# Performance work log

Hardware: AMD Instinct MI355X
Metric: run time of the kernel (lower is better)

## Reference

```python
import jax, jax.numpy as jnp
import numpy as np
from jax import lax
import math

DIM = 64
NUM_HEADS = 8
HEAD_SIZE = DIM // NUM_HEADS  # used only for the 1/sqrt scale


def _depth_conv(x, dw, db, pw, pb):
    # x: [B, C, H, W]; dw: [C, 1, 3, 3] depthwise; pw: [C_out, C] pointwise 1x1
    C = x.shape[1]
    y = lax.conv_general_dilated(
        x, dw, window_strides=(1, 1), padding=[(1, 1), (1, 1)],
        dimension_numbers=("NCHW", "OIHW", "NCHW"), feature_group_count=C)
    y = y + db[None, :, None, None]
    y = jnp.einsum("bchw,oc->bohw", y, pw) + pb[None, :, None, None]
    return y


def setup_inputs() -> dict:
    key = jax.random.key(0)
    ks = jax.random.split(key, 14)
    B, C, H, W = 8, DIM, 256, 256
    inp = {
        "hidden_states": jax.random.normal(ks[0], (B, C, H, W), jnp.float32),
        "ctx": jax.random.normal(ks[1], (B, C, H, W), jnp.float32),
    }
    scale_dw = 1.0 / math.sqrt(9)      # fan_in = 1*3*3 for depthwise
    scale_pw = 1.0 / math.sqrt(C)      # fan_in = C*1*1 for pointwise
    for i, name in enumerate(["q", "k", "v"]):
        k0, k1, k2, k3 = ks[2 + 4 * i: 6 + 4 * i]
        inp[f"{name}_dw"] = jax.random.normal(k0, (C, 1, 3, 3), jnp.float32) * scale_dw
        inp[f"{name}_db"] = jax.random.normal(k1, (C,), jnp.float32) * 0.01
        inp[f"{name}_pw"] = jax.random.normal(k2, (C, C), jnp.float32) * scale_pw
        inp[f"{name}_pb"] = jax.random.normal(k3, (C,), jnp.float32) * 0.01
    return inp


def reference(hidden_states, ctx, q_dw, q_db, q_pw, q_pb,
              k_dw, k_db, k_pw, k_pb, v_dw, v_db, v_pw, v_pb):
    q = _depth_conv(hidden_states, q_dw, q_db, q_pw, q_pb)  # [B,C,H,W]
    k = _depth_conv(ctx, k_dw, k_db, k_pw, k_pb)
    v = _depth_conv(ctx, v_dw, v_db, v_pw, v_pb)
    # permute(0,2,1,3): [B,C,H,W] -> [B,H,C,W]; attention over channels, per row
    qT = q.transpose(0, 2, 1, 3)
    kT = k.transpose(0, 2, 1, 3)
    vT = v.transpose(0, 2, 1, 3)
    scores = jnp.einsum("bhcw,bhdw->bhcd", qT, kT) / math.sqrt(HEAD_SIZE)
    probs = jax.nn.softmax(scores, axis=-1)  # [B,H,C,C]
    out = jnp.einsum("bhcd,bhdw->bhcw", probs, vT)
    return out.transpose(0, 2, 1, 3)  # back to [B,C,H,W]
```

## Files before the change

kernel.cpp:

```cpp
#include <hip/hip_runtime.h>

#define NBATCH 8
#define CH 64
#define HH 256
#define WW 256
#define CK 64
#define NCK (WW / CK)
#define LDP (CK + 4)

__global__ __launch_bounds__(256, 4)
void fused_ca(const float* __restrict__ hid, const float* __restrict__ ctx,
              const float* __restrict__ qdw, const float* __restrict__ qdb,
              const float* __restrict__ qpw, const float* __restrict__ qpb,
              const float* __restrict__ kdw, const float* __restrict__ kdb,
              const float* __restrict__ kpw, const float* __restrict__ kpb,
              const float* __restrict__ vdw, const float* __restrict__ vdb,
              const float* __restrict__ vpw, const float* __restrict__ vpb,
              float* __restrict__ out)
{
    __shared__ float bufA[CH][LDP];
    __shared__ float bufB[CH][LDP];
    __shared__ float ssq[CH], ssk[CH], salpha[CH], sbeta[CH];

    const int tid = threadIdx.x;
    const int wg = (blockIdx.x & 7) * ((int)gridDim.x >> 3) + ((int)blockIdx.x >> 3);
    const int b  = wg >> 8;
    const int h  = wg & 255;

    const int r  = tid >> 2;
    const int g  = tid & 3;
    const int c0 = g * 16;

    const float SCALE = 0.35355339059327373f;

    auto dwconv = [&](const float* __restrict__ src, const float* wgt, float bias,
                      int wc, bool kmode) -> float {
        float acc[16];
        #pragma unroll
        for (int i = 0; i < 16; i++) acc[i] = bias;
        const int w0 = wc * CK + c0 - 1;
        #pragma unroll
        for (int dy = 0; dy < 3; dy++) {
            const int hr = h + dy - 1;
            if (hr < 0 || hr >= HH) continue;
            const float* p = src + (((size_t)b * CH + r) * HH + hr) * WW;
            float t[18];
            #pragma unroll
            for (int j = 0; j < 18; j++) {
                const int w = w0 + j;
                t[j] = (w >= 0 && w < WW) ? p[w] : 0.f;
            }
            #pragma unroll
            for (int dx = 0; dx < 3; dx++) {
                const float wv = wgt[dy * 3 + dx];
                #pragma unroll
                for (int i = 0; i < 16; i++) acc[i] += t[i + dx] * wv;
            }
        }
        float s = 0.f;
        #pragma unroll
        for (int i = 0; i < 16; i++) s += acc[i];
        if (kmode) {
            #pragma unroll
            for (int i = 0; i < 16; i++) bufB[c0 + i][r] = acc[i];
        } else {
            #pragma unroll
            for (int i = 0; i < 16; i++) bufA[r][c0 + i] = acc[i];
        }
        return s;
    };

    float qw[9], kw[9];
    #pragma unroll
    for (int i = 0; i < 9; i++) { qw[i] = qdw[r * 9 + i]; kw[i] = kdw[r * 9 + i]; }
    const float qb = qdb[r], kb = kdb[r];

    float sacc[16];
    #pragma unroll
    for (int i = 0; i < 16; i++) sacc[i] = 0.f;
    float sq_part = 0.f, sk_part = 0.f;

    for (int wc = 0; wc < NCK; wc++) {
        sq_part += dwconv(hid, qw, qb, wc, false);
        sk_part += dwconv(ctx, kw, kb, wc, true);
        __syncthreads();
        #pragma unroll 4
        for (int w = 0; w < CK; w++) {
            const float qv = bufA[r][w];
            #pragma unroll
            for (int i = 0; i < 16; i++) sacc[i] += qv * bufB[w][c0 + i];
        }
        __syncthreads();
    }

    sq_part += __shfl_xor(sq_part, 1);
    sq_part += __shfl_xor(sq_part, 2);
    sk_part += __shfl_xor(sk_part, 1);
    sk_part += __shfl_xor(sk_part, 2);
    if (g == 0) { ssq[r] = sq_part; ssk[r] = sk_part; }

    #pragma unroll
    for (int i = 0; i < 16; i++) bufA[r][c0 + i] = sacc[i];
    __syncthreads();

    {
        float acc[16];
        #pragma unroll
        for (int i = 0; i < 16; i++) acc[i] = 0.f;
        #pragma unroll 4
        for (int e = 0; e < CH; e++) {
            const float wv = qpw[r * CH + e];
            #pragma unroll
            for (int i = 0; i < 16; i++) acc[i] += wv * bufA[e][c0 + i];
        }
        #pragma unroll
        for (int i = 0; i < 16; i++) bufB[r][c0 + i] = acc[i] * SCALE;
    }
    if (tid < CH) {
        float a = 0.f;
        #pragma unroll 4
        for (int e = 0; e < CH; e++) a += qpw[tid * CH + e] * ssq[e];
        salpha[tid] = a;
    } else if (tid < 2 * CH) {
        const int d = tid - CH;
        float a = 0.f;
        #pragma unroll 4
        for (int e = 0; e < CH; e++) a += kpw[d * CH + e] * ssk[e];
        sbeta[d] = a;
    }
    __syncthreads();

    #pragma unroll
    for (int j = 0; j < 4; j++) {
        const float4 kv = *reinterpret_cast<const float4*>(&kpw[r * CH + c0 + 4 * j]);
        bufA[c0 + 4 * j + 0][r] = kv.x;
        bufA[c0 + 4 * j + 1][r] = kv.y;
        bufA[c0 + 4 * j + 2][r] = kv.z;
        bufA[c0 + 4 * j + 3][r] = kv.w;
    }
    __syncthreads();

    float p[16];
    {
        float s[16];
        #pragma unroll
        for (int i = 0; i < 16; i++) s[i] = 0.f;
        #pragma unroll 4
        for (int e = 0; e < CH; e++) {
            const float wv = bufB[r][e];
            #pragma unroll
            for (int i = 0; i < 16; i++) s[i] += wv * bufA[e][c0 + i];
        }
        const float qpbr = qpb[r];
        const float gam  = SCALE * (salpha[r] + 256.f * qpbr);
        const float qs   = SCALE * qpbr;
        #pragma unroll
        for (int i = 0; i < 16; i++)
            s[i] += gam * kpb[c0 + i] + qs * sbeta[c0 + i];
        float m = s[0];
        #pragma unroll
        for (int i = 1; i < 16; i++) m = fmaxf(m, s[i]);
        m = fmaxf(m, __shfl_xor(m, 1));
        m = fmaxf(m, __shfl_xor(m, 2));
        float sum = 0.f;
        #pragma unroll
        for (int i = 0; i < 16; i++) { s[i] = __expf(s[i] - m); sum += s[i]; }
        sum += __shfl_xor(sum, 1);
        sum += __shfl_xor(sum, 2);
        const float inv = 1.f / sum;
        #pragma unroll
        for (int i = 0; i < 16; i++) p[i] = s[i] * inv;
    }
    __syncthreads();

    #pragma unroll
    for (int i = 0; i < 16; i++) bufA[r][c0 + i] = p[i];
    #pragma unroll
    for (int j = 0; j < 4; j++) {
        *reinterpret_cast<float4*>(&bufB[r][c0 + 4 * j]) =
            *reinterpret_cast<const float4*>(&vpw[r * CH + c0 + 4 * j]);
    }
    __syncthreads();

    float macc[16];
    #pragma unroll
    for (int i = 0; i < 16; i++) macc[i] = 0.f;
    float pbd = 0.f;
    #pragma unroll 4
    for (int d = 0; d < CH; d++) {
        const float pv = bufA[r][d];
        pbd += pv * vpb[d];
        #pragma unroll
        for (int i = 0; i < 16; i++) macc[i] += pv * bufB[d][c0 + i];
    }
    __syncthreads();
    #pragma unroll
    for (int i = 0; i < 16; i++) bufB[r][c0 + i] = macc[i];

    float vw[9];
    #pragma unroll
    for (int i = 0; i < 9; i++) vw[i] = vdw[r * 9 + i];
    const float vb = vdb[r];
    __syncthreads();

    for (int wc = 0; wc < NCK; wc++) {
        (void)dwconv(ctx, vw, vb, wc, false);
        __syncthreads();
        float o[16];
        #pragma unroll
        for (int i = 0; i < 16; i++) o[i] = 0.f;
        #pragma unroll 4
        for (int e = 0; e < CH; e++) {
            const float mv = bufB[r][e];
            #pragma unroll
            for (int i = 0; i < 16; i++) o[i] += mv * bufA[e][c0 + i];
        }
        float* po = out + (((size_t)b * CH + r) * HH + h) * WW + wc * CK + c0;
        #pragma unroll
        for (int i = 0; i < 16; i++) po[i] = o[i] + pbd;
        __syncthreads();
    }
}

extern "C" void kernel_launch(void* const* d_in, const int* in_sizes, int n_in,
                              void* d_out, int out_size, void* d_ws, size_t ws_size,
                              hipStream_t stream) {
    const float* hid = (const float*)d_in[0];
    const float* ctx = (const float*)d_in[1];
    const float* qdw = (const float*)d_in[2];
    const float* qdb = (const float*)d_in[3];
    const float* qpw = (const float*)d_in[4];
    const float* qpb = (const float*)d_in[5];
    const float* kdw = (const float*)d_in[6];
    const float* kdb = (const float*)d_in[7];
    const float* kpw = (const float*)d_in[8];
    const float* kpb = (const float*)d_in[9];
    const float* vdw = (const float*)d_in[10];
    const float* vdb = (const float*)d_in[11];
    const float* vpw = (const float*)d_in[12];
    const float* vpb = (const float*)d_in[13];
    float* out = (float*)d_out;

    dim3 grid(NBATCH * HH);
    dim3 block(256);
    fused_ca<<<grid, block, 0, stream>>>(hid, ctx, qdw, qdb, qpw, qpb,
                                         kdw, kdb, kpw, kpb, vdw, vdb, vpw, vpb,
                                         out);
}
```

Measured before the change: 618.9 us.

## Move channel-attention matmuls to bf16x3 MFMA with swizzled LDS layout

Replaces the scalar-FMA Q·K^T accumulation and final M·V output matmul with MFMA 16x16x32 bf16 instructions. Fp32 accuracy is approximated by splitting each value into high and low bf16 parts and issuing three products. Operands are staged in LDS with XOR-swizzled packed layouts, and the depthwise conv loads become vectorized float4. Small weight matmuls now read global weights directly instead of staging through LDS, which saves syncs. In exchange it adds split/pack overhead, drops to 2 blocks per CU in launch bounds, and loses a little precision versus pure fp32.

```diff
diff --git a/kernel.cpp b/kernel.cpp
--- a/kernel.cpp
+++ b/kernel.cpp
@@ -4,11 +4,18 @@
 #define CH 64
 #define HH 256
 #define WW 256
-#define CK 64
-#define NCK (WW / CK)
-#define LDP (CK + 4)
-
-__global__ __launch_bounds__(256, 4)
+
+using f32x4 = __attribute__((ext_vector_type(4))) float;
+using s16x8 = __attribute__((ext_vector_type(8))) short;
+typedef unsigned short ushort_t;
+
+#define SM_BYTES 35072
+#define AQ_OFF 17408
+#define AK_OFF (17408 + 8192)
+#define M_OFF  17408
+#define VEC_OFF 33792
+
+__global__ __launch_bounds__(256, 2)
 void fused_ca(const float* __restrict__ hid, const float* __restrict__ ctx,
               const float* __restrict__ qdw, const float* __restrict__ qdb,
               const float* __restrict__ qpw, const float* __restrict__ qpb,
@@ -18,55 +25,72 @@
               const float* __restrict__ vpw, const float* __restrict__ vpb,
               float* __restrict__ out)
 {
-    __shared__ float bufA[CH][LDP];
-    __shared__ float bufB[CH][LDP];
-    __shared__ float ssq[CH], ssk[CH], salpha[CH], sbeta[CH];
-
-    const int tid = threadIdx.x;
+    __shared__ alignas(16) char sm[SM_BYTES];
+    float* bigf   = (float*)sm;
+    float* ssq    = (float*)(sm + VEC_OFF);
+    float* ssk    = ssq + 64;
+    float* salpha = ssq + 128;
+    float* sbeta  = ssq + 192;
+    float* spbd   = ssq + 256;
+
+    const int tid  = threadIdx.x;
+    const int wid  = tid >> 6;
+    const int lane = tid & 63;
+    const int sl   = lane >> 4;
+
     const int wg = (blockIdx.x & 7) * ((int)gridDim.x >> 3) + ((int)blockIdx.x >> 3);
-    const int b  = wg >> 8;
-    const int h  = wg & 255;
+    const int b  = wg >> 8, h = wg & 255;
 
     const int r  = tid >> 2;
     const int g  = tid & 3;
     const int c0 = g * 16;
-
     const float SCALE = 0.35355339059327373f;
 
-    auto dwconv = [&](const float* __restrict__ src, const float* wgt, float bias,
-                      int wc, bool kmode) -> float {
-        float acc[16];
-        #pragma unroll
-        for (int i = 0; i < 16; i++) acc[i] = bias;
-        const int w0 = wc * CK + c0 - 1;
+    auto pack2 = [](float x, float y) -> unsigned int {
+        return (__float_as_uint(x) >> 16) | (__float_as_uint(y) & 0xFFFF0000u);
+    };
+
+    auto conv8 = [&](const float* __restrict__ src, const float* wgt, float bias,
+                     int wc, int dstoff) -> float {
+        float acc[8];
+        #pragma unroll
+        for (int i = 0; i < 8; i++) acc[i] = bias;
+        const int wb = wc * 32 + g * 8;
+        const float* p0 = src + ((size_t)b * CH + r) * (HH * WW) + wb;
+        const int offL = (wb > 0) ? -1 : 0;
+        const int offR = (wb + 8 < WW) ? 8 : 7;
         #pragma unroll
         for (int dy = 0; dy < 3; dy++) {
             const int hr = h + dy - 1;
             if (hr < 0 || hr >= HH) continue;
-            const float* p = src + (((size_t)b * CH + r) * HH + hr) * WW;
-            float t[18];
-            #pragma unroll
-            for (int j = 0; j < 18; j++) {
-                const int w = w0 + j;
-                t[j] = (w >= 0 && w < WW) ? p[w] : 0.f;
-            }
+            const float* p = p0 + (size_t)hr * WW;
+            const float4 t0 = *(const float4*)p;
+            const float4 t1 = *(const float4*)(p + 4);
+            float tl = p[offL]; if (wb == 0) tl = 0.f;
+            float tr = p[offR]; if (wb + 8 >= WW) tr = 0.f;
+            const float t[10] = {tl, t0.x, t0.y, t0.z, t0.w, t1.x, t1.y, t1.z, t1.w, tr};
             #pragma unroll
             for (int dx = 0; dx < 3; dx++) {
                 const float wv = wgt[dy * 3 + dx];
                 #pragma unroll
-                for (int i = 0; i < 16; i++) acc[i] += t[i + dx] * wv;
+                for (int i = 0; i < 8; i++) acc[i] += t[i + dx] * wv;
             }
         }
         float s = 0.f;
         #pragma unroll
-        for (int i = 0; i < 16; i++) s += acc[i];
-        if (kmode) {
-            #pragma unroll
-            for (int i = 0; i < 16; i++) bufB[c0 + i][r] = acc[i];
-        } else {
-            #pragma unroll
-            for (int i = 0; i < 16; i++) bufA[r][c0 + i] = acc[i];
-        }
+        for (int i = 0; i < 8; i++) s += acc[i];
+        float lo[8];
+        #pragma unroll
+        for (int i = 0; i < 8; i++) {
+            const float hf = __uint_as_float(__float_as_uint(acc[i]) & 0xFFFF0000u);
+            lo[i] = acc[i] - hf;
+        }
+        const uint4 uh = make_uint4(pack2(acc[0], acc[1]), pack2(acc[2], acc[3]),
+                                    pack2(acc[4], acc[5]), pack2(acc[6], acc[7]));
+        const uint4 ul = make_uint4(pack2(lo[0], lo[1]), pack2(lo[2], lo[3]),
+                                    pack2(lo[4], lo[5]), pack2(lo[6], lo[7]));
+        *(uint4*)(sm + dstoff + r * 128 + (((g    ) ^ (r & 7)) << 4)) = uh;
+        *(uint4*)(sm + dstoff + r * 128 + (((g + 4) ^ (r & 7)) << 4)) = ul;
         return s;
     };
 
@@ -75,81 +99,94 @@
     for (int i = 0; i < 9; i++) { qw[i] = qdw[r * 9 + i]; kw[i] = kdw[r * 9 + i]; }
     const float qb = qdb[r], kb = kdb[r];
 
-    float sacc[16];
-    #pragma unroll
-    for (int i = 0; i < 16; i++) sacc[i] = 0.f;
+    f32x4 accT[4];
+    #pragma unroll
+    for (int tn = 0; tn < 4; tn++) accT[tn] = f32x4{0.f, 0.f, 0.f, 0.f};
     float sq_part = 0.f, sk_part = 0.f;
 
-    for (int wc = 0; wc < NCK; wc++) {
-        sq_part += dwconv(hid, qw, qb, wc, false);
-        sk_part += dwconv(ctx, kw, kb, wc, true);
+    for (int wc = 0; wc < 8; wc++) {
+        sq_part += conv8(hid, qw, qb, wc, AQ_OFF);
+        sk_part += conv8(ctx, kw, kb, wc, AK_OFF);
         __syncthreads();
-        #pragma unroll 4
-        for (int w = 0; w < CK; w++) {
-            const float qv = bufA[r][w];
-            #pragma unroll
-            for (int i = 0; i < 16; i++) sacc[i] += qv * bufB[w][c0 + i];
+        const int ra = (wid << 4) + (lane & 15);
+        const s16x8 ah = *(const s16x8*)(sm + AQ_OFF + ra * 128 + (((sl    ) ^ (ra & 7)) << 4));
+        const s16x8 al = *(const s16x8*)(sm + AQ_OFF + ra * 128 + (((sl + 4) ^ (ra & 7)) << 4));
+        #pragma unroll
+        for (int tn = 0; tn < 4; tn++) {
+            const int rb = (tn << 4) + (lane & 15);
+            const s16x8 bh = *(const s16x8*)(sm + AK_OFF + rb * 128 + (((sl    ) ^ (rb & 7)) << 4));
+            const s16x8 bl = *(const s16x8*)(sm + AK_OFF + rb * 128 + (((sl + 4) ^ (rb & 7)) << 4));
+            accT[tn] = __builtin_amdgcn_mfma_f32_16x16x32_bf16(ah, bh, accT[tn], 0, 0, 0);
+            accT[tn] = __builtin_amdgcn_mfma_f32_16x16x32_bf16(ah, bl, accT[tn], 0, 0, 0);
+            accT[tn] = __builtin_amdgcn_mfma_f32_16x16x32_bf16(al, bh, accT[tn], 0, 0, 0);
         }
         __syncthreads();
     }
 
-    sq_part += __shfl_xor(sq_part, 1);
-    sq_part += __shfl_xor(sq_part, 2);
-    sk_part += __shfl_xor(sk_part, 1);
-    sk_part += __shfl_xor(sk_part, 2);
+    sq_part += __shfl_xor(sq_part, 1); sq_part += __shfl_xor(sq_part, 2);
+    sk_part += __shfl_xor(sk_part, 1); sk_part += __shfl_xor(sk_part, 2);
     if (g == 0) { ssq[r] = sq_part; ssk[r] = sk_part; }
 
-    #pragma unroll
-    for (int i = 0; i < 16; i++) bufA[r][c0 + i] = sacc[i];
+    {
+        const int rowb = (wid << 4) + ((lane >> 4) << 2);
+        const int cb = lane & 15;
+        #pragma unroll
+        for (int tn = 0; tn < 4; tn++)
+            #pragma unroll
+            for (int q = 0; q < 4; q++)
+                bigf[(rowb + q) * 68 + tn * 16 + cb] = accT[tn][q];
+    }
     __syncthreads();
 
-    {
-        float acc[16];
-        #pragma unroll
-        for (int i = 0; i < 16; i++) acc[i] = 0.f;
-        #pragma unroll 4
-        for (int e = 0; e < CH; e++) {
-            const float wv = qpw[r * CH + e];
-            #pragma unroll
-            for (int i = 0; i < 16; i++) acc[i] += wv * bufA[e][c0 + i];
-        }
-        #pragma unroll
-        for (int i = 0; i < 16; i++) bufB[r][c0 + i] = acc[i] * SCALE;
-    }
-    if (tid < CH) {
+    float w2a[16];
+    #pragma unroll
+    for (int i = 0; i < 16; i++) w2a[i] = 0.f;
+    #pragma unroll 4
+    for (int e4 = 0; e4 < 16; e4++) {
+        const float4 wq = *(const float4*)&qpw[r * 64 + e4 * 4];
+        const float ws[4] = {wq.x, wq.y, wq.z, wq.w};
+        #pragma unroll
+        for (int j = 0; j < 4; j++)
+            #pragma unroll
+            for (int i = 0; i < 16; i++)
+                w2a[i] += ws[j] * bigf[(e4 * 4 + j) * 68 + c0 + i];
+    }
+    if (tid < 64) {
         float a = 0.f;
         #pragma unroll 4
-        for (int e = 0; e < CH; e++) a += qpw[tid * CH + e] * ssq[e];
+        for (int e = 0; e < 64; e += 4) {
+            const float4 w4 = *(const float4*)&qpw[tid * 64 + e];
+            a += w4.x * ssq[e] + w4.y * ssq[e + 1] + w4.z * ssq[e + 2] + w4.w * ssq[e + 3];
+        }
         salpha[tid] = a;
-    } else if (tid < 2 * CH) {
-        const int d = tid - CH;
+    } else if (tid < 128) {
+        const int d = tid - 64;
         float a = 0.f;
         #pragma unroll 4
-        for (int e = 0; e < CH; e++) a += kpw[d * CH + e] * ssk[e];
+        for (int e = 0; e < 64; e += 4) {
+            const float4 w4 = *(const float4*)&kpw[d * 64 + e];
+            a += w4.x * ssk[e] + w4.y * ssk[e + 1] + w4.z * ssk[e + 2] + w4.w * ssk[e + 3];
+        }
         sbeta[d] = a;
     }
     __syncthreads();
 
     #pragma unroll
-    for (int j = 0; j < 4; j++) {
-        const float4 kv = *reinterpret_cast<const float4*>(&kpw[r * CH + c0 + 4 * j]);
-        bufA[c0 + 4 * j + 0][r] = kv.x;
-        bufA[c0 + 4 * j + 1][r] = kv.y;
-        bufA[c0 + 4 * j + 2][r] = kv.z;
-        bufA[c0 + 4 * j + 3][r] = kv.w;
-    }
-    __syncthreads();
+    for (int i = 0; i < 16; i++) bigf[r * 68 + c0 + i] = w2a[i] * SCALE;
 
     float p[16];
     {
         float s[16];
         #pragma unroll
         for (int i = 0; i < 16; i++) s[i] = 0.f;
-        #pragma unroll 4
-        for (int e = 0; e < CH; e++) {
-            const float wv = bufB[r][e];
-            #pragma unroll
-            for (int i = 0; i < 16; i++) s[i] += wv * bufA[e][c0 + i];
+        #pragma unroll 2
+        for (int e4 = 0; e4 < 16; e4++) {
+            const float4 w4 = *(const float4*)&bigf[r * 68 + e4 * 4];
+            #pragma unroll
+            for (int i = 0; i < 16; i++) {
+                const float4 kv = *(const float4*)&kpw[(c0 + i) * 64 + e4 * 4];
+                s[i] += w4.x * kv.x + w4.y * kv.y + w4.z * kv.z + w4.w * kv.w;
+            }
         }
         const float qpbr = qpb[r];
         const float gam  = SCALE * (salpha[r] + 256.f * qpbr);
@@ -171,53 +208,126 @@
         #pragma unroll
         for (int i = 0; i < 16; i++) p[i] = s[i] * inv;
     }
-    __syncthreads();
-
-    #pragma unroll
-    for (int i = 0; i < 16; i++) bufA[r][c0 + i] = p[i];
-    #pragma unroll
-    for (int j = 0; j < 4; j++) {
-        *reinterpret_cast<float4*>(&bufB[r][c0 + 4 * j]) =
-            *reinterpret_cast<const float4*>(&vpw[r * CH + c0 + 4 * j]);
-    }
-    __syncthreads();
+    #pragma unroll
+    for (int i = 0; i < 16; i++) bigf[r * 68 + c0 + i] = p[i];
 
     float macc[16];
     #pragma unroll
     for (int i = 0; i < 16; i++) macc[i] = 0.f;
     float pbd = 0.f;
-    #pragma unroll 4
-    for (int d = 0; d < CH; d++) {
-        const float pv = bufA[r][d];
-        pbd += pv * vpb[d];
-        #pragma unroll
-        for (int i = 0; i < 16; i++) macc[i] += pv * bufB[d][c0 + i];
-    }
+    #pragma unroll 2
+    for (int d4 = 0; d4 < 16; d4++) {
+        const float4 p4  = *(const float4*)&bigf[r * 68 + d4 * 4];
+        const float4 vb4 = *(const float4*)&vpb[d4 * 4];
+        pbd += p4.x * vb4.x + p4.y * vb4.y + p4.z * vb4.z + p4.w * vb4.w;
+        const float ps[4] = {p4.x, p4.y, p4.z, p4.w};
+        #pragma unroll
+        for (int j = 0; j < 4; j++)
+            #pragma unroll
+            for (int i = 0; i < 16; i++)
+                macc[i] += ps[j] * vpw[(d4 * 4 + j) * 64 + c0 + i];
+    }
+    {
+        float lo[16];
+        #pragma unroll
+        for (int i = 0; i < 16; i++) {
+            const float hf = __uint_as_float(__float_as_uint(macc[i]) & 0xFFFF0000u);
+            lo[i] = macc[i] - hf;
+        }
+        const uint4 u0 = make_uint4(pack2(macc[0], macc[1]), pack2(macc[2], macc[3]),
+                                    pack2(macc[4], macc[5]), pack2(macc[6], macc[7]));
+        const uint4 u1 = make_uint4(pack2(macc[8], macc[9]), pack2(macc[10], macc[11]),
+                                    pack2(macc[12], macc[13]), pack2(macc[14], macc[15]));
+        const uint4 l0 = make_uint4(pack2(lo[0], lo[1]), pack2(lo[2], lo[3]),
+                                    pack2(lo[4], lo[5]), pack2(lo[6], lo[7]));
+        const uint4 l1 = make_uint4(pack2(lo[8], lo[9]), pack2(lo[10], lo[11]),
+                                    pack2(lo[12], lo[13]), pack2(lo[14], lo[15]));
+        *(uint4*)(sm + M_OFF + r * 256 + (((2 * g    ) ^ (r & 15)) << 4)) = u0;
+        *(uint4*)(sm + M_OFF + r * 256 + (((2 * g + 1) ^ (r & 15)) << 4)) = u1;
+        *(uint4*)(sm + M_OFF + r * 256 + (((8 + 2 * g) ^ (r & 15)) << 4)) = l0;
+        *(uint4*)(sm + M_OFF + r * 256 + (((9 + 2 * g) ^ (r & 15)) << 4)) = l1;
+    }
+    if (g == 0) spbd[r] = pbd;
     __syncthreads();
-    #pragma unroll
-    for (int i = 0; i < 16; i++) bufB[r][c0 + i] = macc[i];
 
     float vw[9];
     #pragma unroll
     for (int i = 0; i < 9; i++) vw[i] = vdw[r * 9 + i];
-    const float vb = vdb[r];
-    __syncthreads();
-
-    for (int wc = 0; wc < NCK; wc++) {
-        (void)dwconv(ctx, vw, vb, wc, false);
+    const float vb_ = vdb[r];
+
+    const int ra2 = (wid << 4) + (lane & 15);
+    const s16x8 mh0 = *(const s16x8*)(sm + M_OFF + ra2 * 256 + (((sl     ) ^ (ra2 & 15)) << 4));
+    const s16x8 mh1 = *(const s16x8*)(sm + M_OFF + ra2 * 256 + (((sl +  4) ^ (ra2 & 15)) << 4));
+    const s16x8 ml0 = *(const s16x8*)(sm + M_OFF + ra2 * 256 + (((sl +  8) ^ (ra2 & 15)) << 4));
+    const s16x8 ml1 = *(const s16x8*)(sm + M_OFF + ra2 * 256 + (((sl + 12) ^ (ra2 & 15)) << 4));
+    float pbd4[4];
+    {
+        const int rowb = (wid << 4) + ((lane >> 4) << 2);
+        #pragma unroll
+        for (int q = 0; q < 4; q++) pbd4[q] = spbd[rowb + q];
+    }
+
+    for (int wc = 0; wc < 4; wc++) {
+        {
+            float acc[16];
+            #pragma unroll
+            for (int i = 0; i < 16; i++) acc[i] = vb_;
+            const int wb = wc * 64 + c0;
+            const float* p0 = ctx + ((size_t)b * CH + r) * (HH * WW) + wb;
+            const int offL = (wb > 0) ? -1 : 0;
+            const int offR = (wb + 16 < WW) ? 16 : 15;
+            #pragma unroll
+            for (int dy = 0; dy < 3; dy++) {
+                const int hr = h + dy - 1;
+                if (hr < 0 || hr >= HH) continue;
+                const float* p = p0 + (size_t)hr * WW;
+                const float4 t0 = *(const float4*)p;
+                const float4 t1 = *(const float4*)(p + 4);
+                const float4 t2 = *(const float4*)(p + 8);
+                const float4 t3 = *(const float4*)(p + 12);
+                float tl = p[offL]; if (wb == 0) tl = 0.f;
+                float tr = p[offR]; if (wb + 16 >= WW) tr = 0.f;
+                const float t[18] = {tl, t0.x, t0.y, t0.z, t0.w, t1.x, t1.y, t1.z, t1.w,
+                                     t2.x, t2.y, t2.z, t2.w, t3.x, t3.y, t3.z, t3.w, tr};
+                #pragma unroll
+                for (int dx = 0; dx < 3; dx++) {
+                    const float wv = vw[dy * 3 + dx];
+                    #pragma unroll
+                    for (int i = 0; i < 16; i++) acc[i] += t[i + dx] * wv;
+                }
+            }
+            #pragma unroll
+            for (int i = 0; i < 16; i++) {
+                const int wl = c0 + i;
+                const unsigned int hb = __float_as_uint(acc[i]) & 0xFFFF0000u;
+                const float lf = acc[i] - __uint_as_float(hb);
+                *(ushort_t*)(sm + wl * 256 + ((((r >> 3)    ) ^ (wl & 15)) << 4) + ((r & 7) << 1)) =
+                    (ushort_t)(hb >> 16);
+                *(ushort_t*)(sm + wl * 256 + (((8 + (r >> 3)) ^ (wl & 15)) << 4) + ((r & 7) << 1)) =
+                    (ushort_t)(__float_as_uint(lf) >> 16);
+            }
+        }
         __syncthreads();
-        float o[16];
-        #pragma unroll
-        for (int i = 0; i < 16; i++) o[i] = 0.f;
-        #pragma unroll 4
-        for (int e = 0; e < CH; e++) {
-            const float mv = bufB[r][e];
-            #pragma unroll
-            for (int i = 0; i < 16; i++) o[i] += mv * bufA[e][c0 + i];
-        }
-        float* po = out + (((size_t)b * CH + r) * HH + h) * WW + wc * CK + c0;
-        #pragma unroll
-        for (int i = 0; i < 16; i++) po[i] = o[i] + pbd;
+        const int rowb = (wid << 4) + ((lane >> 4) << 2);
+        #pragma unroll
+        for (int tn = 0; tn < 4; tn++) {
+            const int rb = (tn << 4) + (lane & 15);
+            const s16x8 bh0 = *(const s16x8*)(sm + rb * 256 + (((sl     ) ^ (rb & 15)) << 4));
+            const s16x8 bh1 = *(const s16x8*)(sm + rb * 256 + (((sl +  4) ^ (rb & 15)) << 4));
+            const s16x8 bl0 = *(const s16x8*)(sm + rb * 256 + (((sl +  8) ^ (rb & 15)) << 4));
+            const s16x8 bl1 = *(const s16x8*)(sm + rb * 256 + (((sl + 12) ^ (rb & 15)) << 4));
+            f32x4 a2 = {0.f, 0.f, 0.f, 0.f};
+            a2 = __builtin_amdgcn_mfma_f32_16x16x32_bf16(mh0, bh0, a2, 0, 0, 0);
+            a2 = __builtin_amdgcn_mfma_f32_16x16x32_bf16(mh0, bl0, a2, 0, 0, 0);
+            a2 = __builtin_amdgcn_mfma_f32_16x16x32_bf16(ml0, bh0, a2, 0, 0, 0);
+            a2 = __builtin_amdgcn_mfma_f32_16x16x32_bf16(mh1, bh1, a2, 0, 0, 0);
+            a2 = __builtin_amdgcn_mfma_f32_16x16x32_bf16(mh1, bl1, a2, 0, 0, 0);
+            a2 = __builtin_amdgcn_mfma_f32_16x16x32_bf16(ml1, bh1, a2, 0, 0, 0);
+            float* po = out + (((size_t)b * CH + rowb) * HH + h) * WW + wc * 64 + tn * 16 + (lane & 15);
+            #pragma unroll
+            for (int q = 0; q < 4; q++)
+                po[(size_t)q * HH * WW] = a2[q] + pbd4[q];
+        }
         __syncthreads();
     }
 }
```

Result: slower. 817.6 us (+32.1%).
